# Optimization experiments

Measured on AMD Instinct MI355X. Metric: run time of the kernel, lower is better.

Reference implementation:

```python
import jax, jax.numpy as jnp
import numpy as np

N = 8192
IN_FEATS = 256
OUT_FEATS = 256


def setup_inputs() -> dict:
    key = jax.random.key(0)
    k_adj, k_x, k_att, k_w = jax.random.split(key, 4)
    adjacency = jax.random.randint(k_adj, (N, N), 0, 2, dtype=jnp.int32)
    inputs = jax.random.normal(k_x, (N, IN_FEATS), dtype=jnp.float32)
    attention_projection = jax.random.normal(k_att, (N, N), dtype=jnp.float32)
    # nn.Linear default init scale ~ 1/sqrt(in_feats)
    W = jax.random.normal(k_w, (IN_FEATS, OUT_FEATS), dtype=jnp.float32) / np.sqrt(IN_FEATS)
    b = jnp.zeros((OUT_FEATS,), dtype=jnp.float32)
    return {"adjacency": adjacency, "inputs": inputs,
            "attention_projection": attention_projection, "W": W, "b": b}


def reference(adjacency, inputs, attention_projection, W, b):
    # aggregation_type == 'sum': x = (attention_projection * adjacency) @ inputs
    adj = adjacency.astype(attention_projection.dtype)  # [N, N] dense mask
    x = (attention_projection * adj) @ inputs            # [N, in_feats]
    # LinearLayer with activation='relu'
    x = jax.nn.relu(x @ W + b)                           # [N, out_feats]
    return x
```

## Files before the change

### kernel.cpp

```cpp
#include <hip/hip_runtime.h>

#define K1 8192
#define F 256
#define BM 32
#define BK 64
#define NSTEP (K1 / BK)

typedef __attribute__((ext_vector_type(8))) short bf16x8;
typedef __attribute__((ext_vector_type(4))) float f32x4;

__device__ __forceinline__ unsigned short f2bf(float f) {
  union { float f; unsigned int u; } v; v.f = f;
  unsigned int u = v.u;
  u += 0x7fffu + ((u >> 16) & 1u);
  return (unsigned short)(u >> 16);
}

__device__ __forceinline__ void gload_lds16(const void* g, void* l) {
  __builtin_amdgcn_global_load_lds((const __attribute__((address_space(1))) void*)g,
                                   (__attribute__((address_space(3))) void*)l,
                                   16, 0, 0);
}

__global__ __launch_bounds__(256) void transpose_cvt(const float* __restrict__ in,
                                                     unsigned short* __restrict__ outT,
                                                     int R, int C) {
  __shared__ float tile[32][33];
  const int r0 = blockIdx.x << 5, c0 = blockIdx.y << 5;
  const int t = threadIdx.x;
  const int rr = t >> 3, cc = (t & 7) << 2;
  float4 v = *(const float4*)(in + (size_t)(r0 + rr) * C + c0 + cc);
  tile[rr][cc + 0] = v.x; tile[rr][cc + 1] = v.y;
  tile[rr][cc + 2] = v.z; tile[rr][cc + 3] = v.w;
  __syncthreads();
  ushort4 o;
  o.x = f2bf(tile[cc + 0][rr]);
  o.y = f2bf(tile[cc + 1][rr]);
  o.z = f2bf(tile[cc + 2][rr]);
  o.w = f2bf(tile[cc + 3][rr]);
  *(ushort4*)(outT + (size_t)(c0 + rr) * R + r0 + cc) = o;
}

__global__ __launch_bounds__(512) void gat_main(
    const float* __restrict__ att, const int* __restrict__ adj,
    const unsigned short* __restrict__ Bt, const unsigned short* __restrict__ Wt,
    const float* __restrict__ bias, float* __restrict__ out) {

  __shared__ alignas(16) unsigned short ldsA[2][BM * BK];
  __shared__ alignas(16) unsigned short ldsB[2][F * BK];
  __shared__ alignas(16) unsigned short ldsX[BM * F];

  const int tid = threadIdx.x;
  const int lane = tid & 63;
  const int w = tid >> 6;
  const int rw = w & 1;
  const int colbase = (w >> 1) << 6;
  const int row0 = blockIdx.x * BM;

  const int ar = tid >> 4;
  const int ac4 = tid & 15;
  const int awbyte = ar * 128 + (((ac4 >> 1) ^ (ar & 7)) << 4) + ((ac4 & 1) << 3);
  const size_t aoff = (size_t)(row0 + ar) * K1 + (ac4 << 2);

  f32x4 acc[4];
#pragma unroll
  for (int f = 0; f < 4; ++f) acc[f] = (f32x4){0.f, 0.f, 0.f, 0.f};

  {
    float4 attv = *(const float4*)(att + aoff);
    int4 adjv = *(const int4*)(adj + aoff);
#pragma unroll
    for (int j = 0; j < 4; ++j) {
      const int byteoff = (j << 13) + (tid << 4);
      const int n = byteoff >> 7;
      const int k2 = ((byteoff >> 4) & 7) ^ (n & 7);
      gload_lds16(Bt + ((size_t)n << 13) + (k2 << 3),
                  (char*)&ldsB[0][0] + (j << 13) + (w << 10));
    }
    ushort4 pk;
    pk.x = f2bf(adjv.x ? attv.x : 0.f);
    pk.y = f2bf(adjv.y ? attv.y : 0.f);
    pk.z = f2bf(adjv.z ? attv.z : 0.f);
    pk.w = f2bf(adjv.w ? attv.w : 0.f);
    *(ushort4*)((char*)&ldsA[0][0] + awbyte) = pk;
    __syncthreads();
  }

  int buf = 0;
  for (int t = 0; t < NSTEP; ++t) {
    const int nxt = buf ^ 1;
    const bool has_next = (t + 1 < NSTEP);
    float4 attv; int4 adjv;
    if (has_next) {
      const int kb = (t + 1) * BK;
      attv = *(const float4*)(att + aoff + kb);
      adjv = *(const int4*)(adj + aoff + kb);
#pragma unroll
      for (int j = 0; j < 4; ++j) {
        const int byteoff = (j << 13) + (tid << 4);
        const int n = byteoff >> 7;
        const int k2 = ((byteoff >> 4) & 7) ^ (n & 7);
        gload_lds16(Bt + ((size_t)n << 13) + kb + (k2 << 3),
                    (char*)&ldsB[nxt][0] + (j << 13) + (w << 10));
      }
    }
#pragma unroll
    for (int s = 0; s < 2; ++s) {
      const int r = (rw << 4) + (lane & 15);
      const int k2a = (s << 2) + (lane >> 4);
      bf16x8 afrag = *(const bf16x8*)((char*)&ldsA[buf][0] + r * 128 + ((k2a ^ (r & 7)) << 4));
#pragma unroll
      for (int f = 0; f < 4; ++f) {
        const int n = colbase + (f << 4) + (lane & 15);
        bf16x8 bfrag = *(const bf16x8*)((char*)&ldsB[buf][0] + n * 128 +
                                        ((((s << 2) + (lane >> 4)) ^ (n & 7)) << 4));
        acc[f] = __builtin_amdgcn_mfma_f32_16x16x32_bf16(afrag, bfrag, acc[f], 0, 0, 0);
      }
    }
    if (has_next) {
      ushort4 pk;
      pk.x = f2bf(adjv.x ? attv.x : 0.f);
      pk.y = f2bf(adjv.y ? attv.y : 0.f);
      pk.z = f2bf(adjv.z ? attv.z : 0.f);
      pk.w = f2bf(adjv.w ? attv.w : 0.f);
      *(ushort4*)((char*)&ldsA[nxt][0] + awbyte) = pk;
    }
    __syncthreads();
    buf = nxt;
  }

#pragma unroll
  for (int f = 0; f < 4; ++f) {
#pragma unroll
    for (int b = 0; b < 4; ++b) {
      const int r = (rw << 4) + ((lane >> 4) << 2) + b;
      const int c = colbase + (f << 4) + (lane & 15);
      const int byte = (r << 9) + ((((c >> 3) ^ (r & 7)) << 4)) + ((c & 7) << 1);
      *(unsigned short*)((char*)&ldsX[0] + byte) = f2bf(acc[f][b]);
    }
  }
  __syncthreads();

  f32x4 acc2[4];
#pragma unroll
  for (int f = 0; f < 4; ++f) {
    const float bv = bias[colbase + (f << 4) + (lane & 15)];
    acc2[f] = (f32x4){bv, bv, bv, bv};
  }
#pragma unroll
  for (int s2 = 0; s2 < 8; ++s2) {
    const int r = (rw << 4) + (lane & 15);
    const int kk = (s2 << 5) + ((lane >> 4) << 3);
    bf16x8 a2 = *(const bf16x8*)((char*)&ldsX[0] + (r << 9) + (((kk >> 3) ^ (r & 7)) << 4));
#pragma unroll
    for (int f = 0; f < 4; ++f) {
      const int n = colbase + (f << 4) + (lane & 15);
      bf16x8 w2 = *(const bf16x8*)(Wt + ((size_t)n << 8) + kk);
      acc2[f] = __builtin_amdgcn_mfma_f32_16x16x32_bf16(a2, w2, acc2[f], 0, 0, 0);
    }
  }
#pragma unroll
  for (int f = 0; f < 4; ++f) {
#pragma unroll
    for (int b = 0; b < 4; ++b) {
      const int r = row0 + (rw << 4) + ((lane >> 4) << 2) + b;
      const int c = colbase + (f << 4) + (lane & 15);
      out[(size_t)r * F + c] = fmaxf(acc2[f][b], 0.f);
    }
  }
}

extern "C" void kernel_launch(void* const* d_in, const int* in_sizes, int n_in,
                              void* d_out, int out_size, void* d_ws, size_t ws_size,
                              hipStream_t stream) {
  const int* adj = (const int*)d_in[0];
  const float* x_in = (const float*)d_in[1];
  const float* att = (const float*)d_in[2];
  const float* W = (const float*)d_in[3];
  const float* b = (const float*)d_in[4];
  float* out = (float*)d_out;

  unsigned short* Bt = (unsigned short*)d_ws;
  unsigned short* Wt = (unsigned short*)((char*)d_ws + (size_t)256 * 8192 * 2);

  dim3 g1(K1 / 32, F / 32);
  transpose_cvt<<<g1, 256, 0, stream>>>(x_in, Bt, K1, F);
  dim3 g2(F / 32, F / 32);
  transpose_cvt<<<g2, 256, 0, stream>>>(W, Wt, F, F);
  gat_main<<<K1 / BM, 512, 0, stream>>>(att, adj, Bt, Wt, b, out);
}
```

Baseline: 626.3 us.

## Read B fragments directly from global/L2, shrink row tile, use nontemporal A loads

Removes the LDS staging of the transposed input matrix and has each wave load its B fragments straight from global memory (relying on L2, since Bt is only 4 MB and shared by all blocks). The row tile is halved to 16 and K-step doubled to 128, with a manually unrolled two-stage register prefetch of the attention/adjacency streams, now read with nontemporal loads. Occupancy hint raised to 4 blocks per CU. The intent is to cut LDS traffic and barrier cost and raise occupancy so the kernel streams the 512 MB of att/adj at closer to HBM bandwidth. The cost is much more L2 traffic for B, because every block rereads all of Bt and there are twice as many blocks.

```diff
diff --git a/kernel.cpp b/kernel.cpp
--- a/kernel.cpp
+++ b/kernel.cpp
@@ -1,25 +1,20 @@
 #include <hip/hip_runtime.h>
 
-#define K1 8192
+#define NROW 8192
 #define F 256
-#define BM 32
-#define BK 64
-#define NSTEP (K1 / BK)
+#define BM 16
+#define BK 128
+#define NSTEP (NROW / BK)
 
 typedef __attribute__((ext_vector_type(8))) short bf16x8;
 typedef __attribute__((ext_vector_type(4))) float f32x4;
+typedef __attribute__((ext_vector_type(4))) int i32x4;
 
 __device__ __forceinline__ unsigned short f2bf(float f) {
   union { float f; unsigned int u; } v; v.f = f;
   unsigned int u = v.u;
   u += 0x7fffu + ((u >> 16) & 1u);
   return (unsigned short)(u >> 16);
-}
-
-__device__ __forceinline__ void gload_lds16(const void* g, void* l) {
-  __builtin_amdgcn_global_load_lds((const __attribute__((address_space(1))) void*)g,
-                                   (__attribute__((address_space(3))) void*)l,
-                                   16, 0, 0);
 }
 
 __global__ __launch_bounds__(256) void transpose_cvt(const float* __restrict__ in,
@@ -41,131 +36,120 @@
   *(ushort4*)(outT + (size_t)(c0 + rr) * R + r0 + cc) = o;
 }
 
-__global__ __launch_bounds__(512) void gat_main(
+__global__ __launch_bounds__(512, 4) void gat_main(
     const float* __restrict__ att, const int* __restrict__ adj,
     const unsigned short* __restrict__ Bt, const unsigned short* __restrict__ Wt,
     const float* __restrict__ bias, float* __restrict__ out) {
 
   __shared__ alignas(16) unsigned short ldsA[2][BM * BK];
-  __shared__ alignas(16) unsigned short ldsB[2][F * BK];
   __shared__ alignas(16) unsigned short ldsX[BM * F];
 
   const int tid = threadIdx.x;
   const int lane = tid & 63;
   const int w = tid >> 6;
-  const int rw = w & 1;
-  const int colbase = (w >> 1) << 6;
+  const int colbase = w << 5;
   const int row0 = blockIdx.x * BM;
 
-  const int ar = tid >> 4;
-  const int ac4 = tid & 15;
-  const int awbyte = ar * 128 + (((ac4 >> 1) ^ (ar & 7)) << 4) + ((ac4 & 1) << 3);
-  const size_t aoff = (size_t)(row0 + ar) * K1 + (ac4 << 2);
+  const int ar = tid >> 5;
+  const int ac = tid & 31;
+  const int awbyte = ar * 256 + ((((ac >> 1) ^ (ar & 7))) << 4) + ((ac & 1) << 3);
+  const float* ap = att + (size_t)(row0 + ar) * NROW + (ac << 2);
+  const int*   jp = adj + (size_t)(row0 + ar) * NROW + (ac << 2);
 
-  f32x4 acc[4];
+  const int r = lane & 15;
+  const int hi = lane >> 4;
+
+  f32x4 acc[2];
+  acc[0] = (f32x4){0.f, 0.f, 0.f, 0.f};
+  acc[1] = (f32x4){0.f, 0.f, 0.f, 0.f};
+
+  auto loadA = [&](int t, f32x4& fv, i32x4& jv) {
+    fv = __builtin_nontemporal_load((const f32x4*)(ap + (size_t)t * BK));
+    jv = __builtin_nontemporal_load((const i32x4*)(jp + (size_t)t * BK));
+  };
+  auto stage = [&](unsigned short* bufA, const f32x4& fv, const i32x4& jv) {
+    ushort4 pk;
+    pk.x = f2bf(jv.x ? fv.x : 0.f);
+    pk.y = f2bf(jv.y ? fv.y : 0.f);
+    pk.z = f2bf(jv.z ? fv.z : 0.f);
+    pk.w = f2bf(jv.w ? fv.w : 0.f);
+    *(ushort4*)((char*)bufA + awbyte) = pk;
+  };
+  auto compute = [&](const unsigned short* bufA, int kb) {
 #pragma unroll
-  for (int f = 0; f < 4; ++f) acc[f] = (f32x4){0.f, 0.f, 0.f, 0.f};
+    for (int ks = 0; ks < 4; ++ks) {
+      const int kk = (ks << 2) + hi;
+      bf16x8 afrag = *(const bf16x8*)((const char*)bufA + r * 256 + ((kk ^ (r & 7)) << 4));
+      const int kg = kb + (ks << 5) + (hi << 3);
+#pragma unroll
+      for (int nt = 0; nt < 2; ++nt) {
+        const int n = colbase + (nt << 4) + r;
+        bf16x8 bfrag = *(const bf16x8*)(Bt + ((size_t)n << 13) + kg);
+        acc[nt] = __builtin_amdgcn_mfma_f32_16x16x32_bf16(afrag, bfrag, acc[nt], 0, 0, 0);
+      }
+    }
+  };
 
-  {
-    float4 attv = *(const float4*)(att + aoff);
-    int4 adjv = *(const int4*)(adj + aoff);
-#pragma unroll
-    for (int j = 0; j < 4; ++j) {
-      const int byteoff = (j << 13) + (tid << 4);
-      const int n = byteoff >> 7;
-      const int k2 = ((byteoff >> 4) & 7) ^ (n & 7);
-      gload_lds16(Bt + ((size_t)n << 13) + (k2 << 3),
-                  (char*)&ldsB[0][0] + (j << 13) + (w << 10));
-    }
-    ushort4 pk;
-    pk.x = f2bf(adjv.x ? attv.x : 0.f);
-    pk.y = f2bf(adjv.y ? attv.y : 0.f);
-    pk.z = f2bf(adjv.z ? attv.z : 0.f);
-    pk.w = f2bf(adjv.w ? attv.w : 0.f);
-    *(ushort4*)((char*)&ldsA[0][0] + awbyte) = pk;
+  f32x4 fa, fb; i32x4 ja, jb;
+  loadA(0, fa, ja);
+  loadA(1, fb, jb);
+  stage(ldsA[0], fa, ja);
+  __syncthreads();
+
+#pragma unroll 1
+  for (int t = 0; t < NSTEP - 2; t += 2) {
+    loadA(t + 2, fa, ja);
+    compute(ldsA[0], t * BK);
+    stage(ldsA[1], fb, jb);
+    __syncthreads();
+    loadA(t + 3, fb, jb);
+    compute(ldsA[1], (t + 1) * BK);
+    stage(ldsA[0], fa, ja);
     __syncthreads();
   }
-
-  int buf = 0;
-  for (int t = 0; t < NSTEP; ++t) {
-    const int nxt = buf ^ 1;
-    const bool has_next = (t + 1 < NSTEP);
-    float4 attv; int4 adjv;
-    if (has_next) {
-      const int kb = (t + 1) * BK;
-      attv = *(const float4*)(att + aoff + kb);
-      adjv = *(const int4*)(adj + aoff + kb);
-#pragma unroll
-      for (int j = 0; j < 4; ++j) {
-        const int byteoff = (j << 13) + (tid << 4);
-        const int n = byteoff >> 7;
-        const int k2 = ((byteoff >> 4) & 7) ^ (n & 7);
-        gload_lds16(Bt + ((size_t)n << 13) + kb + (k2 << 3),
-                    (char*)&ldsB[nxt][0] + (j << 13) + (w << 10));
-      }
-    }
-#pragma unroll
-    for (int s = 0; s < 2; ++s) {
-      const int r = (rw << 4) + (lane & 15);
-      const int k2a = (s << 2) + (lane >> 4);
-      bf16x8 afrag = *(const bf16x8*)((char*)&ldsA[buf][0] + r * 128 + ((k2a ^ (r & 7)) << 4));
-#pragma unroll
-      for (int f = 0; f < 4; ++f) {
-        const int n = colbase + (f << 4) + (lane & 15);
-        bf16x8 bfrag = *(const bf16x8*)((char*)&ldsB[buf][0] + n * 128 +
-                                        ((((s << 2) + (lane >> 4)) ^ (n & 7)) << 4));
-        acc[f] = __builtin_amdgcn_mfma_f32_16x16x32_bf16(afrag, bfrag, acc[f], 0, 0, 0);
-      }
-    }
-    if (has_next) {
-      ushort4 pk;
-      pk.x = f2bf(adjv.x ? attv.x : 0.f);
-      pk.y = f2bf(adjv.y ? attv.y : 0.f);
-      pk.z = f2bf(adjv.z ? attv.z : 0.f);
-      pk.w = f2bf(adjv.w ? attv.w : 0.f);
-      *(ushort4*)((char*)&ldsA[nxt][0] + awbyte) = pk;
-    }
-    __syncthreads();
-    buf = nxt;
-  }
+  compute(ldsA[0], (NSTEP - 2) * BK);
+  stage(ldsA[1], fb, jb);
+  __syncthreads();
+  compute(ldsA[1], (NSTEP - 1) * BK);
 
 #pragma unroll
-  for (int f = 0; f < 4; ++f) {
+  for (int nt = 0; nt < 2; ++nt) {
 #pragma unroll
     for (int b = 0; b < 4; ++b) {
-      const int r = (rw << 4) + ((lane >> 4) << 2) + b;
-      const int c = colbase + (f << 4) + (lane & 15);
-      const int byte = (r << 9) + ((((c >> 3) ^ (r & 7)) << 4)) + ((c & 7) << 1);
-      *(unsigned short*)((char*)&ldsX[0] + byte) = f2bf(acc[f][b]);
+      const int xr = (hi << 2) + b;
+      const int c = colbase + (nt << 4) + r;
+      const int kk2 = c >> 3;
+      const int byte = xr * 512 + ((kk2 ^ (xr & 7)) << 4) + ((c & 7) << 1);
+      *(unsigned short*)((char*)ldsX + byte) = f2bf(acc[nt][b]);
     }
   }
   __syncthreads();
 
-  f32x4 acc2[4];
+  f32x4 acc2[2];
 #pragma unroll
-  for (int f = 0; f < 4; ++f) {
-    const float bv = bias[colbase + (f << 4) + (lane & 15)];
-    acc2[f] = (f32x4){bv, bv, bv, bv};
+  for (int nt = 0; nt < 2; ++nt) {
+    const float bv = bias[colbase + (nt << 4) + r];
+    acc2[nt] = (f32x4){bv, bv, bv, bv};
   }
 #pragma unroll
-  for (int s2 = 0; s2 < 8; ++s2) {
-    const int r = (rw << 4) + (lane & 15);
-    const int kk = (s2 << 5) + ((lane >> 4) << 3);
-    bf16x8 a2 = *(const bf16x8*)((char*)&ldsX[0] + (r << 9) + (((kk >> 3) ^ (r & 7)) << 4));
+  for (int ks2 = 0; ks2 < 8; ++ks2) {
+    const int kk2 = (ks2 << 2) + hi;
+    bf16x8 a2 = *(const bf16x8*)((char*)ldsX + r * 512 + ((kk2 ^ (r & 7)) << 4));
+    const int kg = (ks2 << 5) + (hi << 3);
 #pragma unroll
-    for (int f = 0; f < 4; ++f) {
-      const int n = colbase + (f << 4) + (lane & 15);
-      bf16x8 w2 = *(const bf16x8*)(Wt + ((size_t)n << 8) + kk);
-      acc2[f] = __builtin_amdgcn_mfma_f32_16x16x32_bf16(a2, w2, acc2[f], 0, 0, 0);
+    for (int nt = 0; nt < 2; ++nt) {
+      const int n = colbase + (nt << 4) + r;
+      bf16x8 w2 = *(const bf16x8*)(Wt + ((size_t)n << 8) + kg);
+      acc2[nt] = __builtin_amdgcn_mfma_f32_16x16x32_bf16(a2, w2, acc2[nt], 0, 0, 0);
     }
   }
 #pragma unroll
-  for (int f = 0; f < 4; ++f) {
+  for (int nt = 0; nt < 2; ++nt) {
 #pragma unroll
     for (int b = 0; b < 4; ++b) {
-      const int r = row0 + (rw << 4) + ((lane >> 4) << 2) + b;
-      const int c = colbase + (f << 4) + (lane & 15);
-      out[(size_t)r * F + c] = fmaxf(acc2[f][b], 0.f);
+      const int rr = row0 + (hi << 2) + b;
+      const int c = colbase + (nt << 4) + r;
+      out[(size_t)rr * F + c] = fmaxf(acc2[nt][b], 0.f);
     }
   }
 }
@@ -183,9 +167,9 @@
   unsigned short* Bt = (unsigned short*)d_ws;
   unsigned short* Wt = (unsigned short*)((char*)d_ws + (size_t)256 * 8192 * 2);
 
-  dim3 g1(K1 / 32, F / 32);
-  transpose_cvt<<<g1, 256, 0, stream>>>(x_in, Bt, K1, F);
+  dim3 g1(NROW / 32, F / 32);
+  transpose_cvt<<<g1, 256, 0, stream>>>(x_in, Bt, NROW, F);
   dim3 g2(F / 32, F / 32);
   transpose_cvt<<<g2, 256, 0, stream>>>(W, Wt, F, F);
-  gat_main<<<K1 / BM, 512, 0, stream>>>(att, adj, Bt, Wt, b, out);
+  gat_main<<<NROW / BM, 512, 0, stream>>>(att, adj, Bt, Wt, b, out);
 }
```

New measurement: 677.2 us. 8.1% more time.
